# Performance work log

Hardware: AMD Instinct MI355X
Metric: run time of the kernel (lower is better)

The kernel has to match this reference:

```python
import jax, jax.numpy as jnp
from jax import lax
import numpy as np

CH = 16      # channel_n
HID = 128    # update MLP width


def setup_inputs() -> dict:
    key = jax.random.key(0)
    ks = jax.random.split(key, 7)
    B, H, W = 4, 224, 224
    x = jax.random.uniform(ks[0], (B, CH, H, W), dtype=jnp.float32)
    # perception: Conv2d(16 -> 48, 3x3, pad 1, no bias), OIHW
    w_percep = jax.random.normal(ks[1], (CH * 3, CH, 3, 3), jnp.float32) * 0.05
    # update MLP: 1x1 convs == pointwise linears over channels
    w1 = jax.random.normal(ks[2], (HID, CH * 3), jnp.float32) * 0.05
    b1 = jax.random.normal(ks[3], (HID,), jnp.float32) * 0.01
    w2 = jax.random.normal(ks[4], (HID, HID), jnp.float32) * 0.05
    b2 = jax.random.normal(ks[5], (HID,), jnp.float32) * 0.01
    w3 = jax.random.normal(ks[6], (CH, HID), jnp.float32) * 0.05  # no bias
    return {"x": x, "w_percep": w_percep, "w1": w1, "b1": b1,
            "w2": w2, "b2": b2, "w3": w3, "steps": 40}


def reference(x, w_percep, w1, b1, w2, b2, w3, steps):
    dn = ("NCHW", "OIHW", "NCHW")

    def step(x, _):
        # 3x3 perception conv, same padding  -> [B, 48, H, W]
        p = lax.conv_general_dilated(x, w_percep, (1, 1), "SAME",
                                     dimension_numbers=dn)
        # pointwise conv-MLP (1x1 convs as channel einsums)
        h = jax.nn.relu(jnp.einsum("bchw,oc->bohw", p, w1) + b1[None, :, None, None])
        h = jax.nn.relu(jnp.einsum("bchw,oc->bohw", h, w2) + b2[None, :, None, None])
        dx = jnp.einsum("bchw,oc->bohw", h, w3)
        # residual update + clamp to [0, 1] (eval mode: no fire mask)
        return jnp.clip(x + dx, 0.0, 1.0), None

    x, _ = lax.scan(step, x, None, length=steps)
    return x
```

## Files before the change

kernel.cpp:

```cpp
#include <hip/hip_runtime.h>


typedef __attribute__((ext_vector_type(8))) short short8;
typedef __attribute__((ext_vector_type(4))) float float4v;

#define MFMA16(a, b, c) __builtin_amdgcn_mfma_f32_16x16x32_bf16((a), (b), (c), 0, 0, 0)

__device__ __forceinline__ short f2bf(float f) {
  unsigned u = __builtin_bit_cast(unsigned, f);
  return (short)((u + 0x8000u) >> 16);
}

__device__ __forceinline__ void async16(const void* g, void* l) {
  __builtin_amdgcn_global_load_lds((const __attribute__((address_space(1))) void*)g,
                                   (__attribute__((address_space(3))) void*)l,
                                   16, 0, 0);
}

__device__ __forceinline__ void sync_lds() {
  asm volatile("s_waitcnt lgkmcnt(0)\n\ts_barrier" ::: "memory");
}

#define WS_WE    0
#define WS_W2    43008
#define WS_W3    77824
#define WS_B1    82944
#define WS_B2    83456
#define WS_X32A  83968
#define WS_X32B  12929024
#define WS_X16A  25774080
#define WS_X16B  32196608

__global__ void prep_x(const float* __restrict__ x, float* __restrict__ x32,
                       short* __restrict__ x16) {
  int i = blockIdx.x * 256 + threadIdx.x;
  int w = i % 224;
  int h = (i / 224) % 224;
  int c = (i / 50176) & 15;
  int bb = i / 802816;
  float v = x[i];
  int o = ((bb * 224 + h) * 224 + w) * 16 + c;
  x32[o] = v;
  x16[o] = f2bf(v);
}

__global__ void prep_w(const float* __restrict__ wp, const float* __restrict__ w1,
                       const float* __restrict__ b1, const float* __restrict__ w2,
                       const float* __restrict__ b2, const float* __restrict__ w3,
                       short* __restrict__ wE, short* __restrict__ w2t,
                       short* __restrict__ w3t, float* __restrict__ b1p,
                       float* __restrict__ b2p) {
  int i = blockIdx.x * 256 + threadIdx.x;
  if (i < 21504) {
    int o = i / 168, k = i % 168;
    float v = 0.f;
    if (k < 144) {
      int off = k >> 4, c = k & 15;
      for (int c3 = 0; c3 < 48; ++c3)
        v += w1[o * 48 + c3] * wp[c3 * 144 + c * 9 + off];
    }
    wE[i] = f2bf(v);
  } else if (i < 38912) {
    int j = i - 21504;
    int n = j / 136, kk = j % 136;
    float v = 0.f;
    if (kk < 128) { int ch = 16 * (kk & 7) + (kk >> 3); v = w2[n * 128 + ch]; }
    w2t[j] = f2bf(v);
  } else if (i < 41472) {
    int j = i - 38912;
    float v = 0.f;
    if (j < 2176) {
      int n = j / 136, kk = j % 136;
      if (kk < 128) { int ch = 16 * (kk & 7) + (kk >> 3); v = w3[n * 128 + ch]; }
    }
    w3t[j] = f2bf(v);
  } else if (i < 41600) {
    int p = i - 41472;
    b1p[p] = b1[16 * (p & 7) + (p >> 3)];
  } else {
    int p = i - 41600;
    b2p[p] = b2[16 * (p & 7) + (p >> 3)];
  }
}

template <bool LAST>
__global__ __launch_bounds__(256, 2) void ca_step(
    const short* __restrict__ wEg, const short* __restrict__ w2g,
    const short* __restrict__ w3g, const float* __restrict__ b1p,
    const float* __restrict__ b2p, const float* __restrict__ xs32,
    const short* __restrict__ xs16, float* __restrict__ xd32,
    short* __restrict__ xd16, float* __restrict__ dout) {
  __shared__ short sXH[4 * 3616];
  __shared__ short sBUF[2 * 2 * 2176];
  __shared__ short sH2[2 * 2 * 2176];

  const int tid = threadIdx.x;
  const int lane = tid & 63;
  const int wv = tid >> 6;
  const int c16 = lane & 15;
  const int q = lane >> 4;
  const int q8 = q * 8;
  const int qh = q >> 1;
  const int c0 = (q & 1) * 8;

  const int blk = blockIdx.x;
  const int b = blk / 112;
  const int h0 = (blk % 112) * 2;

  const short8 z8 = {0, 0, 0, 0, 0, 0, 0, 0};
  for (int t = wv; t < 28; t += 4) {
    int hr = t / 7, ck = t % 7;
    int hh = h0 - 1 + hr;
    char* l = (char*)sXH + hr * 7232 + 32 + ck * 1024;
    if (hh >= 0 && hh < 224) {
      const char* g = (const char*)xs16 + ((size_t)(b * 224 + hh) * 224) * 32 + ck * 1024;
      async16(g + lane * 16, l);
    } else {
      *(short8*)(l + lane * 16) = z8;
    }
  }
  if (tid < 16) {
    int hr = tid >> 2, wch = tid & 3;
    int colb = (wch < 2) ? 0 : 225;
    *(short8*)((char*)sXH + hr * 7232 + colb * 32 + (wch & 1) * 16) = z8;
  }

  if (wv < 2) {
    short8 wf[5][8];
#pragma unroll
    for (int kc = 0; kc < 5; ++kc)
#pragma unroll
      for (int nt = 0; nt < 8; ++nt)
        wf[kc][nt] = *(const short8*)(wEg + (nt * 16 + c16) * 168 + kc * 32 + q8);
    const float4v bA = *(const float4v*)(b1p + c16 * 8);
    const float4v bB = *(const float4v*)(b1p + c16 * 8 + 4);

    __syncthreads();

    for (int j = 0; j < 16; ++j) {
      if (j < 14) {
        const int t = 2 * j + wv;
        const int rr = t / 14, cb = (t % 14) * 16;
        const int hbase = (rr * 226 + cb) * 16;
        float4v acc[8];
#pragma unroll
        for (int nt = 0; nt < 8; ++nt) acc[nt] = (float4v){0.f, 0.f, 0.f, 0.f};
#pragma unroll
        for (int kc = 0; kc < 5; ++kc) {
          int off = kc * 2 + qh;
          if (off > 8) off = 8;
          int dy = (off * 11) >> 5;
          int dxx = off - dy * 3;
          short8 a = *(const short8*)(sXH + hbase + (dy * 226 + dxx + c16) * 16 + c0);
#pragma unroll
          for (int nt = 0; nt < 8; ++nt) acc[nt] = MFMA16(a, wf[kc][nt], acc[nt]);
        }
        short* dst = sBUF + ((j & 1) * 2 + wv) * 2176;
#pragma unroll
        for (int r = 0; r < 4; ++r) {
          short8 pk;
#pragma unroll
          for (int nt = 0; nt < 8; ++nt) {
            float v = acc[nt][r] + ((nt < 4) ? bA[nt] : bB[nt - 4]);
            pk[nt] = f2bf(fmaxf(v, 0.f));
          }
          *(short8*)(dst + (q * 4 + r) * 136 + c16 * 8) = pk;
        }
      }
      sync_lds();
    }
  } else {
    short8 w2f[4][8];
    short8 w3f[4];
#pragma unroll
    for (int kc = 0; kc < 4; ++kc)
#pragma unroll
      for (int nt = 0; nt < 8; ++nt)
        w2f[kc][nt] = *(const short8*)(w2g + (nt * 16 + c16) * 136 + kc * 32 + q8);
#pragma unroll
    for (int kc = 0; kc < 4; ++kc)
      w3f[kc] = *(const short8*)(w3g + c16 * 136 + kc * 32 + q8);
    const float4v bA = *(const float4v*)(b2p + c16 * 8);
    const float4v bB = *(const float4v*)(b2p + c16 * 8 + 4);

    const int g = wv - 2;

    __syncthreads();

    for (int j = 0; j < 16; ++j) {
      float xres[4];
      int cb3 = 0, hglob3 = 0;
      if (j >= 2) {
        const int t3 = 2 * (j - 2) + g;
        cb3 = (t3 % 14) * 16; hglob3 = h0 + t3 / 14;
#pragma unroll
        for (int r = 0; r < 4; ++r) {
          size_t pix = (size_t)(b * 224 + hglob3) * 224 + cb3 + q * 4 + r;
          xres[r] = xs32[pix * 16 + c16];
        }
      }
      if (j >= 1 && j <= 14) {
        const short* src = sBUF + (((j - 1) & 1) * 2 + g) * 2176;
        float4v acc2[8];
#pragma unroll
        for (int nt = 0; nt < 8; ++nt) acc2[nt] = (float4v){0.f, 0.f, 0.f, 0.f};
#pragma unroll
        for (int kc = 0; kc < 4; ++kc) {
          short8 a = *(const short8*)(src + c16 * 136 + kc * 32 + q8);
#pragma unroll
          for (int nt = 0; nt < 8; ++nt) acc2[nt] = MFMA16(a, w2f[kc][nt], acc2[nt]);
        }
        short* dsth2 = sH2 + ((j & 1) * 2 + g) * 2176;
#pragma unroll
        for (int r = 0; r < 4; ++r) {
          short8 pk;
#pragma unroll
          for (int nt = 0; nt < 8; ++nt) {
            float v = acc2[nt][r] + ((nt < 4) ? bA[nt] : bB[nt - 4]);
            pk[nt] = f2bf(fmaxf(v, 0.f));
          }
          *(short8*)(dsth2 + (q * 4 + r) * 136 + c16 * 8) = pk;
        }
      }
      if (j >= 2) {
        const short* srch2 = sH2 + (((j - 1) & 1) * 2 + g) * 2176;
        float4v acc3 = (float4v){0.f, 0.f, 0.f, 0.f};
#pragma unroll
        for (int kc = 0; kc < 4; ++kc) {
          short8 a = *(const short8*)(srch2 + c16 * 136 + kc * 32 + q8);
          acc3 = MFMA16(a, w3f[kc], acc3);
        }
#pragma unroll
        for (int r = 0; r < 4; ++r) {
          int col = cb3 + q * 4 + r;
          size_t pix = (size_t)(b * 224 + hglob3) * 224 + col;
          float v = xres[r] + acc3[r];
          v = fminf(fmaxf(v, 0.f), 1.f);
          if (LAST) {
            dout[((size_t)(b * 16 + c16) * 224 + hglob3) * 224 + col] = v;
          } else {
            xd32[pix * 16 + c16] = v;
            xd16[pix * 16 + c16] = f2bf(v);
          }
        }
      }
      sync_lds();
    }
  }
}

extern "C" void kernel_launch(void* const* d_in, const int* in_sizes, int n_in,
                              void* d_out, int out_size, void* d_ws, size_t ws_size,
                              hipStream_t stream) {
  const float* x  = (const float*)d_in[0];
  const float* wp = (const float*)d_in[1];
  const float* w1 = (const float*)d_in[2];
  const float* b1 = (const float*)d_in[3];
  const float* w2 = (const float*)d_in[4];
  const float* b2 = (const float*)d_in[5];
  const float* w3 = (const float*)d_in[6];

  char* ws = (char*)d_ws;
  short* wEg = (short*)(ws + WS_WE);
  short* w2g = (short*)(ws + WS_W2);
  short* w3g = (short*)(ws + WS_W3);
  float* b1p = (float*)(ws + WS_B1);
  float* b2p = (float*)(ws + WS_B2);
  float* X32[2] = {(float*)(ws + WS_X32A), (float*)(ws + WS_X32B)};
  short* X16[2] = {(short*)(ws + WS_X16A), (short*)(ws + WS_X16B)};

  prep_x<<<12544, 256, 0, stream>>>(x, X32[0], X16[0]);
  prep_w<<<163, 256, 0, stream>>>(wp, w1, b1, w2, b2, w3, wEg, w2g, w3g, b1p, b2p);

  for (int s = 0; s < 39; ++s) {
    int sb = s & 1;
    ca_step<false><<<448, 256, 0, stream>>>(wEg, w2g, w3g, b1p, b2p,
                                            X32[sb], X16[sb],
                                            X32[1 - sb], X16[1 - sb], nullptr);
  }
  ca_step<true><<<448, 256, 0, stream>>>(wEg, w2g, w3g, b1p, b2p,
                                         X32[1], X16[1],
                                         X32[0], X16[0], (float*)d_out);
}
```

Baseline: 1.120 ms.

## Split MLP stages across eight waves by output-channel slices

Result: faster. 1.007 ms (-10.1%).

```diff
diff --git a/kernel.cpp b/kernel.cpp
--- a/kernel.cpp
+++ b/kernel.cpp
@@ -3,12 +3,24 @@
 
 typedef __attribute__((ext_vector_type(8))) short short8;
 typedef __attribute__((ext_vector_type(4))) float float4v;
+typedef __attribute__((ext_vector_type(2))) float float2v;
 
 #define MFMA16(a, b, c) __builtin_amdgcn_mfma_f32_16x16x32_bf16((a), (b), (c), 0, 0, 0)
 
 __device__ __forceinline__ short f2bf(float f) {
   unsigned u = __builtin_bit_cast(unsigned, f);
   return (short)((u + 0x8000u) >> 16);
+}
+
+__device__ __forceinline__ unsigned pk2bf(float a, float b) {
+#if __has_builtin(__builtin_amdgcn_cvt_pk_bf16_f32)
+  typedef __attribute__((ext_vector_type(2))) __bf16 bf2;
+  bf2 r = __builtin_amdgcn_cvt_pk_bf16_f32(a, b);
+  return __builtin_bit_cast(unsigned, r);
+#else
+  unsigned ua = __builtin_bit_cast(unsigned, a), ub = __builtin_bit_cast(unsigned, b);
+  return ((ua + 0x8000u) >> 16) | (((ub + 0x8000u) >> 16) << 16);
+#endif
 }
 
 __device__ __forceinline__ void async16(const void* g, void* l) {
@@ -84,7 +96,7 @@
 }
 
 template <bool LAST>
-__global__ __launch_bounds__(256, 2) void ca_step(
+__global__ __launch_bounds__(512, 4) void ca_step(
     const short* __restrict__ wEg, const short* __restrict__ w2g,
     const short* __restrict__ w3g, const float* __restrict__ b1p,
     const float* __restrict__ b2p, const float* __restrict__ xs32,
@@ -108,7 +120,7 @@
   const int h0 = (blk % 112) * 2;
 
   const short8 z8 = {0, 0, 0, 0, 0, 0, 0, 0};
-  for (int t = wv; t < 28; t += 4) {
+  for (int t = wv; t < 28; t += 8) {
     int hr = t / 7, ck = t % 7;
     int hh = h0 - 1 + hr;
     char* l = (char*)sXH + hr * 7232 + 32 + ck * 1024;
@@ -125,72 +137,76 @@
     *(short8*)((char*)sXH + hr * 7232 + colb * 32 + (wch & 1) * 16) = z8;
   }
 
-  if (wv < 2) {
-    short8 wf[5][8];
+  if (wv < 4) {
+    const int wq = wv;
+    short8 wf[5][2];
 #pragma unroll
     for (int kc = 0; kc < 5; ++kc)
 #pragma unroll
-      for (int nt = 0; nt < 8; ++nt)
-        wf[kc][nt] = *(const short8*)(wEg + (nt * 16 + c16) * 168 + kc * 32 + q8);
-    const float4v bA = *(const float4v*)(b1p + c16 * 8);
-    const float4v bB = *(const float4v*)(b1p + c16 * 8 + 4);
+      for (int n = 0; n < 2; ++n)
+        wf[kc][n] = *(const short8*)(wEg + ((2 * wq + n) * 16 + c16) * 168 + kc * 32 + q8);
+    const float2v bH = *(const float2v*)(b1p + c16 * 8 + 2 * wq);
 
     __syncthreads();
 
     for (int j = 0; j < 16; ++j) {
       if (j < 14) {
-        const int t = 2 * j + wv;
-        const int rr = t / 14, cb = (t % 14) * 16;
-        const int hbase = (rr * 226 + cb) * 16;
-        float4v acc[8];
-#pragma unroll
-        for (int nt = 0; nt < 8; ++nt) acc[nt] = (float4v){0.f, 0.f, 0.f, 0.f};
+        const int t0 = 2 * j, t1 = t0 + 1;
+        const int hb0 = ((t0 / 14) * 226 + (t0 % 14) * 16) * 16;
+        const int hb1 = ((t1 / 14) * 226 + (t1 % 14) * 16) * 16;
+        float4v acc[2][2];
+#pragma unroll
+        for (int tt = 0; tt < 2; ++tt)
+#pragma unroll
+          for (int n = 0; n < 2; ++n) acc[tt][n] = (float4v){0.f, 0.f, 0.f, 0.f};
 #pragma unroll
         for (int kc = 0; kc < 5; ++kc) {
           int off = kc * 2 + qh;
           if (off > 8) off = 8;
           int dy = (off * 11) >> 5;
           int dxx = off - dy * 3;
-          short8 a = *(const short8*)(sXH + hbase + (dy * 226 + dxx + c16) * 16 + c0);
-#pragma unroll
-          for (int nt = 0; nt < 8; ++nt) acc[nt] = MFMA16(a, wf[kc][nt], acc[nt]);
-        }
-        short* dst = sBUF + ((j & 1) * 2 + wv) * 2176;
-#pragma unroll
-        for (int r = 0; r < 4; ++r) {
-          short8 pk;
-#pragma unroll
-          for (int nt = 0; nt < 8; ++nt) {
-            float v = acc[nt][r] + ((nt < 4) ? bA[nt] : bB[nt - 4]);
-            pk[nt] = f2bf(fmaxf(v, 0.f));
-          }
-          *(short8*)(dst + (q * 4 + r) * 136 + c16 * 8) = pk;
+          const int ao = (dy * 226 + dxx + c16) * 16 + c0;
+          short8 a0 = *(const short8*)(sXH + hb0 + ao);
+          short8 a1 = *(const short8*)(sXH + hb1 + ao);
+#pragma unroll
+          for (int n = 0; n < 2; ++n) {
+            acc[0][n] = MFMA16(a0, wf[kc][n], acc[0][n]);
+            acc[1][n] = MFMA16(a1, wf[kc][n], acc[1][n]);
+          }
+        }
+#pragma unroll
+        for (int tt = 0; tt < 2; ++tt) {
+          short* dst = sBUF + ((j & 1) * 2 + tt) * 2176;
+#pragma unroll
+          for (int r = 0; r < 4; ++r) {
+            unsigned d = pk2bf(fmaxf(acc[tt][0][r] + bH[0], 0.f),
+                               fmaxf(acc[tt][1][r] + bH[1], 0.f));
+            *(unsigned*)(dst + (q * 4 + r) * 136 + c16 * 8 + 2 * wq) = d;
+          }
         }
       }
       sync_lds();
     }
   } else {
-    short8 w2f[4][8];
+    const int g = wv - 4;
+    short8 w2f[4][2];
     short8 w3f[4];
 #pragma unroll
     for (int kc = 0; kc < 4; ++kc)
 #pragma unroll
-      for (int nt = 0; nt < 8; ++nt)
-        w2f[kc][nt] = *(const short8*)(w2g + (nt * 16 + c16) * 136 + kc * 32 + q8);
+      for (int n = 0; n < 2; ++n)
+        w2f[kc][n] = *(const short8*)(w2g + ((2 * g + n) * 16 + c16) * 136 + kc * 32 + q8);
 #pragma unroll
     for (int kc = 0; kc < 4; ++kc)
       w3f[kc] = *(const short8*)(w3g + c16 * 136 + kc * 32 + q8);
-    const float4v bA = *(const float4v*)(b2p + c16 * 8);
-    const float4v bB = *(const float4v*)(b2p + c16 * 8 + 4);
-
-    const int g = wv - 2;
+    const float2v bG = *(const float2v*)(b2p + c16 * 8 + 2 * g);
 
     __syncthreads();
 
     for (int j = 0; j < 16; ++j) {
       float xres[4];
       int cb3 = 0, hglob3 = 0;
-      if (j >= 2) {
+      if (g < 2 && j >= 2) {
         const int t3 = 2 * (j - 2) + g;
         cb3 = (t3 % 14) * 16; hglob3 = h0 + t3 / 14;
 #pragma unroll
@@ -200,29 +216,35 @@
         }
       }
       if (j >= 1 && j <= 14) {
-        const short* src = sBUF + (((j - 1) & 1) * 2 + g) * 2176;
-        float4v acc2[8];
-#pragma unroll
-        for (int nt = 0; nt < 8; ++nt) acc2[nt] = (float4v){0.f, 0.f, 0.f, 0.f};
+        const short* srcA = sBUF + (((j - 1) & 1) * 2 + 0) * 2176;
+        const short* srcB = sBUF + (((j - 1) & 1) * 2 + 1) * 2176;
+        float4v acc2[2][2];
+#pragma unroll
+        for (int tt = 0; tt < 2; ++tt)
+#pragma unroll
+          for (int n = 0; n < 2; ++n) acc2[tt][n] = (float4v){0.f, 0.f, 0.f, 0.f};
 #pragma unroll
         for (int kc = 0; kc < 4; ++kc) {
-          short8 a = *(const short8*)(src + c16 * 136 + kc * 32 + q8);
-#pragma unroll
-          for (int nt = 0; nt < 8; ++nt) acc2[nt] = MFMA16(a, w2f[kc][nt], acc2[nt]);
-        }
-        short* dsth2 = sH2 + ((j & 1) * 2 + g) * 2176;
-#pragma unroll
-        for (int r = 0; r < 4; ++r) {
-          short8 pk;
-#pragma unroll
-          for (int nt = 0; nt < 8; ++nt) {
-            float v = acc2[nt][r] + ((nt < 4) ? bA[nt] : bB[nt - 4]);
-            pk[nt] = f2bf(fmaxf(v, 0.f));
-          }
-          *(short8*)(dsth2 + (q * 4 + r) * 136 + c16 * 8) = pk;
+          short8 aA = *(const short8*)(srcA + c16 * 136 + kc * 32 + q8);
+          short8 aB = *(const short8*)(srcB + c16 * 136 + kc * 32 + q8);
+#pragma unroll
+          for (int n = 0; n < 2; ++n) {
+            acc2[0][n] = MFMA16(aA, w2f[kc][n], acc2[0][n]);
+            acc2[1][n] = MFMA16(aB, w2f[kc][n], acc2[1][n]);
+          }
+        }
+#pragma unroll
+        for (int tt = 0; tt < 2; ++tt) {
+          short* dsth2 = sH2 + ((j & 1) * 2 + tt) * 2176;
+#pragma unroll
+          for (int r = 0; r < 4; ++r) {
+            unsigned d = pk2bf(fmaxf(acc2[tt][0][r] + bG[0], 0.f),
+                               fmaxf(acc2[tt][1][r] + bG[1], 0.f));
+            *(unsigned*)(dsth2 + (q * 4 + r) * 136 + c16 * 8 + 2 * g) = d;
+          }
         }
       }
-      if (j >= 2) {
+      if (g < 2 && j >= 2) {
         const short* srch2 = sH2 + (((j - 1) & 1) * 2 + g) * 2176;
         float4v acc3 = (float4v){0.f, 0.f, 0.f, 0.f};
 #pragma unroll
@@ -274,11 +296,11 @@
 
   for (int s = 0; s < 39; ++s) {
     int sb = s & 1;
-    ca_step<false><<<448, 256, 0, stream>>>(wEg, w2g, w3g, b1p, b2p,
+    ca_step<false><<<448, 512, 0, stream>>>(wEg, w2g, w3g, b1p, b2p,
                                             X32[sb], X16[sb],
                                             X32[1 - sb], X16[1 - sb], nullptr);
   }
-  ca_step<true><<<448, 256, 0, stream>>>(wEg, w2g, w3g, b1p, b2p,
+  ca_step<true><<<448, 512, 0, stream>>>(wEg, w2g, w3g, b1p, b2p,
                                          X32[1], X16[1],
                                          X32[0], X16[0], (float*)d_out);
 }
```
